# Optimization experiments

Hardware: AMD Instinct MI355X
Metric: run time of the kernel (lower is better)

Reference implementation:

```python
import jax, jax.numpy as jnp
import numpy as np

B = 131072   # batch of state samples
H = 512      # hidden width of reconstructed subnets
EPS_DIAG = 0.1  # diagonal regularization ensuring M is invertible


def setup_inputs() -> dict:
    key = jax.random.key(0)
    ks = jax.random.split(key, 20)
    f32 = jnp.float32
    inp = {
        "q":      jax.random.normal(ks[0], (B, 3), dtype=f32),
        "q_dot":  jax.random.normal(ks[1], (B, 3), dtype=f32),
        "s":      jax.random.normal(ks[2], (B, 3), dtype=f32),
        "s_Ddot": jax.random.normal(ks[3], (B, 3), dtype=f32),
        "tau":    jax.random.normal(ks[4], (B, 3), dtype=f32),
        # viscous / coulomb friction coefficients (f_v1..3, f_c1..3)
        "fv": jnp.full((3,), 0.05, dtype=f32),
        "fc": jnp.full((3,), 0.05, dtype=f32),
        # Mass net: 3 -> H -> 9
        "W1m": jax.random.normal(ks[5], (3, H), dtype=f32) * 0.1,
        "b1m": jnp.zeros((H,), dtype=f32),
        "W2m": jax.random.normal(ks[6], (H, 9), dtype=f32) * 0.05,
        "b2m": jnp.zeros((9,), dtype=f32),
        # Gravity net: 3 -> H -> 3
        "W1g": jax.random.normal(ks[7], (3, H), dtype=f32) * 0.1,
        "b1g": jnp.zeros((H,), dtype=f32),
        "W2g": jax.random.normal(ks[8], (H, 3), dtype=f32) * 0.05,
        "b2g": jnp.zeros((3,), dtype=f32),
        # KAB net: concat(q, s, s_Ddot)=9 -> H -> 3
        "W1k": jax.random.normal(ks[9], (9, H), dtype=f32) * 0.1,
        "b1k": jnp.zeros((H,), dtype=f32),
        "W2k": jax.random.normal(ks[10], (H, 3), dtype=f32) * 0.05,
        "b2k": jnp.zeros((3,), dtype=f32),
    }
    return inp


def reference(q, q_dot, s, s_Ddot, tau, fv, fc,
              W1m, b1m, W2m, b2m,
              W1g, b1g, W2g, b2g,
              W1k, b1k, W2k, b2k) -> jnp.ndarray:
    # Mass matrix net -> [B,3,3], made SPD-ish so inv(M) is well defined
    hm = jnp.tanh(q @ W1m + b1m)                       # [B,H]
    Mraw = (hm @ W2m + b2m).reshape(-1, 3, 3)          # [B,3,3]
    M = jnp.einsum('bij,bkj->bik', Mraw, Mraw) + EPS_DIAG * jnp.eye(3, dtype=q.dtype)

    # Gravity net -> [B,3]
    hg = jnp.tanh(q @ W1g + b1g)
    G = hg @ W2g + b2g

    # KAB net on concat(q, s, s_Ddot) -> [B,3]
    x = jnp.concatenate([q, s, s_Ddot], axis=-1)       # [B,9]
    hk = jnp.tanh(x @ W1k + b1k)
    KAB = hk @ W2k + b2k

    # diag(fv) @ q_dot and diag(fc) @ sign(q_dot) are elementwise scalings
    rhs = -G + KAB - fv * q_dot - fc * jnp.sign(q_dot) + tau  # [B,3]

    # q_Ddot = inv(M) @ rhs  (solve is the same math, fewer ops)
    q_Ddot = jnp.linalg.solve(M, rhs[..., None]).squeeze(-1)  # [B,3]
    return q_Ddot
```

## Files before the change

kernel.cpp:

```cpp
#include <hip/hip_runtime.h>
#include <math.h>

#define HDIM 512
#define NCH1 96
#define NCH2 48
#define EPS_DIAG 0.1f

typedef __fp16 h2 __attribute__((ext_vector_type(2)));
typedef __fp16 h8 __attribute__((ext_vector_type(8)));
typedef float f32x4 __attribute__((ext_vector_type(4)));
typedef unsigned int u32x4 __attribute__((ext_vector_type(4)));

__device__ __forceinline__ h2 f2h2(float a, float b) {
    return __builtin_amdgcn_cvt_pkrtz(a, b);
}

__device__ __forceinline__ h2 tanh2(h2 x) {
    const h2 HI = {(__fp16)2.0f,        (__fp16)2.0f};
    const h2 LO = {(__fp16)-2.0f,       (__fp16)-2.0f};
    const h2 C0 = {(__fp16)0.993654f,   (__fp16)0.993654f};
    const h2 C1 = {(__fp16)-0.29463f,   (__fp16)-0.29463f};
    const h2 C2 = {(__fp16)0.0695331f,  (__fp16)0.0695331f};
    const h2 C3 = {(__fp16)-0.00696328f,(__fp16)-0.00696328f};
    h2 t = __builtin_elementwise_min(__builtin_elementwise_max(x, LO), HI);
    h2 u = t * t;
    h2 p = __builtin_elementwise_fma(C3, u, C2);
    p = __builtin_elementwise_fma(p, u, C1);
    p = __builtin_elementwise_fma(p, u, C0);
    return t * p;
}

__device__ __forceinline__ float w1c_at(int k, int hid,
    const float* W1m, const float* b1m, const float* W1g, const float* b1g,
    const float* W1k, const float* b1k)
{
    if (hid < 512)  { if (k < 3) return W1m[k*HDIM + hid]; if (k == 9) return b1m[hid]; return 0.f; }
    if (hid < 1024) { const int h = hid - 512;
                      if (k < 3) return W1g[k*HDIM + h];  if (k == 9) return b1g[h];  return 0.f; }
    const int h = hid - 1024;
    if (k < 9) return W1k[k*HDIM + h]; if (k == 9) return b1k[h]; return 0.f;
}

__global__ void pack_frags(const float* __restrict__ W1m, const float* __restrict__ b1m,
                           const float* __restrict__ W2m,
                           const float* __restrict__ W1g, const float* __restrict__ b1g,
                           const float* __restrict__ W2g,
                           const float* __restrict__ W1k, const float* __restrict__ b1k,
                           const float* __restrict__ W2k,
                           __fp16* __restrict__ frag)
{
    const int tid = blockIdx.x * blockDim.x + threadIdx.x;
    if (tid >= (NCH1 + NCH2) * 64) return;
    const int c = tid >> 6, l = tid & 63;
    const int m = l & 15, kq = l >> 4;
    __fp16* dst = frag + (size_t)tid * 8;
    if (c < NCH1) {
        const int t = c >> 1, phase = c & 1;
        const int hid = 32*t + 8*(m >> 2) + (m & 3) + 4*phase;
        #pragma unroll
        for (int j = 0; j < 8; ++j) {
            const int k = kq*8 + j;
            dst[j] = (__fp16)((k < 10) ? w1c_at(k, hid, W1m, b1m, W1g, b1g, W1k, b1k) : 0.f);
        }
    } else {
        const int t = c - NCH1;
        #pragma unroll
        for (int j = 0; j < 8; ++j) {
            const int hid = 32*t + kq*8 + j;
            float v = 0.f;
            if (hid < 512)       { if (m < 9)             v = W2m[hid*9 + m]; }
            else if (hid < 1024) { if (m >= 9 && m < 12)  v = W2g[(hid-512)*3 + (m-9)]; }
            else                 { if (m >= 12 && m < 15) v = W2k[(hid-1024)*3 + (m-12)]; }
            dst[j] = (__fp16)v;
        }
    }
}

__global__ __launch_bounds__(256, 4) void dyn_kernel(
    const __fp16* __restrict__ frag,
    const float* __restrict__ q, const float* __restrict__ q_dot,
    const float* __restrict__ s, const float* __restrict__ s_Ddot,
    const float* __restrict__ tau,
    const float* __restrict__ fv, const float* __restrict__ fc,
    const float* __restrict__ b2m, const float* __restrict__ b2g,
    const float* __restrict__ b2k,
    float* __restrict__ out, int n)
{
    __shared__ float ebuf[4][32][20];

    const int lane = threadIdx.x & 63;
    const int w    = threadIdx.x >> 6;
    const int col  = lane & 15;
    const int quad = lane >> 4;
    const int base32 = (blockIdx.x * 4 + w) * 32;

    h8 ax0, ax1;
    {
        int sm = base32 + col; if (sm >= n) sm = n - 1;
        const float q0 = q[3*sm+0], q1 = q[3*sm+1], q2 = q[3*sm+2];
        const float s0 = s[3*sm+0], s1 = s[3*sm+1], s2 = s[3*sm+2];
        const float d0 = s_Ddot[3*sm+0], d1 = s_Ddot[3*sm+1], d2 = s_Ddot[3*sm+2];
        const bool z0 = (quad == 0), z1 = (quad == 1);
        ax0[0] = (__fp16)(z0 ? q0 : (z1 ? d2  : 0.f));
        ax0[1] = (__fp16)(z0 ? q1 : (z1 ? 1.f : 0.f));
        ax0[2] = (__fp16)(z0 ? q2 : 0.f);
        ax0[3] = (__fp16)(z0 ? s0 : 0.f);
        ax0[4] = (__fp16)(z0 ? s1 : 0.f);
        ax0[5] = (__fp16)(z0 ? s2 : 0.f);
        ax0[6] = (__fp16)(z0 ? d0 : 0.f);
        ax0[7] = (__fp16)(z0 ? d1 : 0.f);
    }
    {
        int sm = base32 + 16 + col; if (sm >= n) sm = n - 1;
        const float q0 = q[3*sm+0], q1 = q[3*sm+1], q2 = q[3*sm+2];
        const float s0 = s[3*sm+0], s1 = s[3*sm+1], s2 = s[3*sm+2];
        const float d0 = s_Ddot[3*sm+0], d1 = s_Ddot[3*sm+1], d2 = s_Ddot[3*sm+2];
        const bool z0 = (quad == 0), z1 = (quad == 1);
        ax1[0] = (__fp16)(z0 ? q0 : (z1 ? d2  : 0.f));
        ax1[1] = (__fp16)(z0 ? q1 : (z1 ? 1.f : 0.f));
        ax1[2] = (__fp16)(z0 ? q2 : 0.f);
        ax1[3] = (__fp16)(z0 ? s0 : 0.f);
        ax1[4] = (__fp16)(z0 ? s1 : 0.f);
        ax1[5] = (__fp16)(z0 ? s2 : 0.f);
        ax1[6] = (__fp16)(z0 ? d0 : 0.f);
        ax1[7] = (__fp16)(z0 ? d1 : 0.f);
    }

    const f32x4 zero4 = {0.f, 0.f, 0.f, 0.f};
    f32x4 acc0 = zero4, acc1 = zero4;

    const h8* p1 = (const h8*)frag + lane;
    const h8* p2 = (const h8*)frag + (size_t)NCH1 * 64 + lane;

#define BODY(W1A, W1B, W2V) do {                                              \
        f32x4 pa0 = __builtin_amdgcn_mfma_f32_16x16x32_f16((W1A), ax0, zero4, 0, 0, 0); \
        f32x4 pb0 = __builtin_amdgcn_mfma_f32_16x16x32_f16((W1B), ax0, zero4, 0, 0, 0); \
        f32x4 pa1 = __builtin_amdgcn_mfma_f32_16x16x32_f16((W1A), ax1, zero4, 0, 0, 0); \
        f32x4 pb1 = __builtin_amdgcn_mfma_f32_16x16x32_f16((W1B), ax1, zero4, 0, 0, 0); \
        u32x4 uv;                                                             \
        uv[0] = __builtin_bit_cast(unsigned int, tanh2(f2h2(pa0[0], pa0[1]))); \
        uv[1] = __builtin_bit_cast(unsigned int, tanh2(f2h2(pa0[2], pa0[3]))); \
        uv[2] = __builtin_bit_cast(unsigned int, tanh2(f2h2(pb0[0], pb0[1]))); \
        uv[3] = __builtin_bit_cast(unsigned int, tanh2(f2h2(pb0[2], pb0[3]))); \
        acc0 = __builtin_amdgcn_mfma_f32_16x16x32_f16((W2V), __builtin_bit_cast(h8, uv), acc0, 0, 0, 0); \
        uv[0] = __builtin_bit_cast(unsigned int, tanh2(f2h2(pa1[0], pa1[1]))); \
        uv[1] = __builtin_bit_cast(unsigned int, tanh2(f2h2(pa1[2], pa1[3]))); \
        uv[2] = __builtin_bit_cast(unsigned int, tanh2(f2h2(pb1[0], pb1[1]))); \
        uv[3] = __builtin_bit_cast(unsigned int, tanh2(f2h2(pb1[2], pb1[3]))); \
        acc1 = __builtin_amdgcn_mfma_f32_16x16x32_f16((W2V), __builtin_bit_cast(h8, uv), acc1, 0, 0, 0); \
    } while (0)

    h8 a0 = p1[0], b0 = p1[64], c0 = p2[0];
    int t = 0;
    for (; t < NCH2 - 2; t += 2) {
        h8 a1 = p1[128], b1 = p1[192], c1 = p2[64];
        p1 += 256; p2 += 128;
        BODY(a0, b0, c0);
        a0 = p1[0]; b0 = p1[64]; c0 = p2[0];
        BODY(a1, b1, c1);
    }
    {
        h8 a1 = p1[128], b1 = p1[192], c1 = p2[64];
        BODY(a0, b0, c0);
        BODY(a1, b1, c1);
    }
#undef BODY

    *(f32x4*)(&ebuf[w][col][4*quad])      = acc0;
    *(f32x4*)(&ebuf[w][16 + col][4*quad]) = acc1;
    asm volatile("s_waitcnt lgkmcnt(0)" ::: "memory");

    if (lane < 32) {
        const int i = base32 + lane;
        if (i < n) {
            const float* R = ebuf[w][lane];
            const float bM0 = R[0]  + b2m[0], bM1 = R[1]  + b2m[1], bM2 = R[2]  + b2m[2];
            const float bM3 = R[3]  + b2m[3], bM4 = R[4]  + b2m[4], bM5 = R[5]  + b2m[5];
            const float bM6 = R[6]  + b2m[6], bM7 = R[7]  + b2m[7], bM8 = R[8]  + b2m[8];
            const float bG0 = R[9]  + b2g[0], bG1 = R[10] + b2g[1], bG2 = R[11] + b2g[2];
            const float bK0 = R[12] + b2k[0], bK1 = R[13] + b2k[1], bK2 = R[14] + b2k[2];

            const float m00 = bM0*bM0 + bM1*bM1 + bM2*bM2 + EPS_DIAG;
            const float m01 = bM0*bM3 + bM1*bM4 + bM2*bM5;
            const float m02 = bM0*bM6 + bM1*bM7 + bM2*bM8;
            const float m11 = bM3*bM3 + bM4*bM4 + bM5*bM5 + EPS_DIAG;
            const float m12 = bM3*bM6 + bM4*bM7 + bM5*bM8;
            const float m22 = bM6*bM6 + bM7*bM7 + bM8*bM8 + EPS_DIAG;

            const float qd0 = q_dot[3*i+0], qd1 = q_dot[3*i+1], qd2 = q_dot[3*i+2];
            const float t0 = tau[3*i+0], t1 = tau[3*i+1], t2 = tau[3*i+2];
            const float fv0 = fv[0], fv1 = fv[1], fv2 = fv[2];
            const float fc0 = fc[0], fc1 = fc[1], fc2 = fc[2];
            const float sg0 = (qd0 > 0.f) ? 1.f : ((qd0 < 0.f) ? -1.f : 0.f);
            const float sg1 = (qd1 > 0.f) ? 1.f : ((qd1 < 0.f) ? -1.f : 0.f);
            const float sg2 = (qd2 > 0.f) ? 1.f : ((qd2 < 0.f) ? -1.f : 0.f);
            const float r0 = -bG0 + bK0 - fv0*qd0 - fc0*sg0 + t0;
            const float r1 = -bG1 + bK1 - fv1*qd1 - fc1*sg1 + t1;
            const float r2 = -bG2 + bK2 - fv2*qd2 - fc2*sg2 + t2;

            const float c00 = m11*m22 - m12*m12;
            const float c01 = m02*m12 - m01*m22;
            const float c02 = m01*m12 - m02*m11;
            const float det = m00*c00 + m01*c01 + m02*c02;
            const float idet = 1.0f / det;
            const float i11 = m00*m22 - m02*m02;
            const float i12 = m01*m02 - m00*m12;
            const float i22 = m00*m11 - m01*m01;

            out[3*i+0] = (c00*r0 + c01*r1 + c02*r2) * idet;
            out[3*i+1] = (c01*r0 + i11*r1 + i12*r2) * idet;
            out[3*i+2] = (c02*r0 + i12*r1 + i22*r2) * idet;
        }
    }
}

extern "C" void kernel_launch(void* const* d_in, const int* in_sizes, int n_in,
                              void* d_out, int out_size, void* d_ws, size_t ws_size,
                              hipStream_t stream) {
    const float* q      = (const float*)d_in[0];
    const float* q_dot  = (const float*)d_in[1];
    const float* s      = (const float*)d_in[2];
    const float* s_Ddot = (const float*)d_in[3];
    const float* tau    = (const float*)d_in[4];
    const float* fv     = (const float*)d_in[5];
    const float* fc     = (const float*)d_in[6];
    const float* W1m    = (const float*)d_in[7];
    const float* b1m    = (const float*)d_in[8];
    const float* W2m    = (const float*)d_in[9];
    const float* b2m    = (const float*)d_in[10];
    const float* W1g    = (const float*)d_in[11];
    const float* b1g    = (const float*)d_in[12];
    const float* W2g    = (const float*)d_in[13];
    const float* b2g    = (const float*)d_in[14];
    const float* W1k    = (const float*)d_in[15];
    const float* b1k    = (const float*)d_in[16];
    const float* W2k    = (const float*)d_in[17];
    const float* b2k    = (const float*)d_in[18];
    float* out = (float*)d_out;
    __fp16* frag = (__fp16*)d_ws;

    const int n = in_sizes[0] / 3;

    pack_frags<<<((NCH1 + NCH2) * 64 + 255) / 256, 256, 0, stream>>>(
        W1m, b1m, W2m, W1g, b1g, W2g, W1k, b1k, W2k, frag);

    const int blocks = (n + 127) / 128;
    dyn_kernel<<<blocks, 256, 0, stream>>>(frag, q, q_dot, s, s_Ddot, tau, fv, fc,
                                           b2m, b2g, b2k, out, n);
}
```

Measured before the change: 129.3 us.

## Split hidden dimension across wave pairs and reduce partial outputs via LDS

Each pair of waves now shares one 32-sample tile. Each wave in the pair processes half of the hidden chunks, and the two partial second-layer accumulators are summed through shared memory before the solve. Blocks now cover 64 samples instead of 128, so the grid doubles, and launch bounds are raised to 8 blocks per CU to shorten each wave's serial MFMA/tanh chain and raise parallelism. The cost is a __syncthreads, extra LDS traffic, a second input load per sample, and tighter register limits.

Measured after the change: 131.4 us. Within noise of the previous version (+1.6%).

```diff
diff --git a/kernel.cpp b/kernel.cpp
--- a/kernel.cpp
+++ b/kernel.cpp
@@ -4,6 +4,7 @@
 #define HDIM 512
 #define NCH1 96
 #define NCH2 48
+#define NCHH 24
 #define EPS_DIAG 0.1f
 
 typedef __fp16 h2 __attribute__((ext_vector_type(2)));
@@ -76,7 +77,7 @@
     }
 }
 
-__global__ __launch_bounds__(256, 4) void dyn_kernel(
+__global__ __launch_bounds__(256, 8) void dyn_kernel(
     const __fp16* __restrict__ frag,
     const float* __restrict__ q, const float* __restrict__ q_dot,
     const float* __restrict__ s, const float* __restrict__ s_Ddot,
@@ -86,13 +87,16 @@
     const float* __restrict__ b2k,
     float* __restrict__ out, int n)
 {
-    __shared__ float ebuf[4][32][20];
+    __shared__ float bufA[2][32][20];
+    __shared__ float bufB[2][32][20];
 
     const int lane = threadIdx.x & 63;
     const int w    = threadIdx.x >> 6;
+    const int pair = w >> 1;
+    const int half = w & 1;
     const int col  = lane & 15;
     const int quad = lane >> 4;
-    const int base32 = (blockIdx.x * 4 + w) * 32;
+    const int base32 = blockIdx.x * 64 + pair * 32;
 
     h8 ax0, ax1;
     {
@@ -129,8 +133,8 @@
     const f32x4 zero4 = {0.f, 0.f, 0.f, 0.f};
     f32x4 acc0 = zero4, acc1 = zero4;
 
-    const h8* p1 = (const h8*)frag + lane;
-    const h8* p2 = (const h8*)frag + (size_t)NCH1 * 64 + lane;
+    const h8* p1 = (const h8*)frag + lane + (size_t)half * (48 * 64);
+    const h8* p2 = (const h8*)frag + (size_t)NCH1 * 64 + lane + (size_t)half * (NCHH * 64);
 
 #define BODY(W1A, W1B, W2V) do {                                              \
         f32x4 pa0 = __builtin_amdgcn_mfma_f32_16x16x32_f16((W1A), ax0, zero4, 0, 0, 0); \
@@ -152,7 +156,7 @@
 
     h8 a0 = p1[0], b0 = p1[64], c0 = p2[0];
     int t = 0;
-    for (; t < NCH2 - 2; t += 2) {
+    for (; t < NCHH - 2; t += 2) {
         h8 a1 = p1[128], b1 = p1[192], c1 = p2[64];
         p1 += 256; p2 += 128;
         BODY(a0, b0, c0);
@@ -166,19 +170,33 @@
     }
 #undef BODY
 
-    *(f32x4*)(&ebuf[w][col][4*quad])      = acc0;
-    *(f32x4*)(&ebuf[w][16 + col][4*quad]) = acc1;
-    asm volatile("s_waitcnt lgkmcnt(0)" ::: "memory");
-
-    if (lane < 32) {
+    {
+        float (*mybuf)[32][20] = half ? bufB : bufA;
+        *(f32x4*)(&mybuf[pair][col][4*quad])      = acc0;
+        *(f32x4*)(&mybuf[pair][16 + col][4*quad]) = acc1;
+    }
+    __syncthreads();
+
+    if (half == 1 && lane < 32) {
         const int i = base32 + lane;
         if (i < n) {
-            const float* R = ebuf[w][lane];
-            const float bM0 = R[0]  + b2m[0], bM1 = R[1]  + b2m[1], bM2 = R[2]  + b2m[2];
-            const float bM3 = R[3]  + b2m[3], bM4 = R[4]  + b2m[4], bM5 = R[5]  + b2m[5];
-            const float bM6 = R[6]  + b2m[6], bM7 = R[7]  + b2m[7], bM8 = R[8]  + b2m[8];
-            const float bG0 = R[9]  + b2g[0], bG1 = R[10] + b2g[1], bG2 = R[11] + b2g[2];
-            const float bK0 = R[12] + b2k[0], bK1 = R[13] + b2k[1], bK2 = R[14] + b2k[2];
+            const float* RA = bufA[pair][lane];
+            const float* RB = bufB[pair][lane];
+            const float bM0 = RA[0]  + RB[0]  + b2m[0];
+            const float bM1 = RA[1]  + RB[1]  + b2m[1];
+            const float bM2 = RA[2]  + RB[2]  + b2m[2];
+            const float bM3 = RA[3]  + RB[3]  + b2m[3];
+            const float bM4 = RA[4]  + RB[4]  + b2m[4];
+            const float bM5 = RA[5]  + RB[5]  + b2m[5];
+            const float bM6 = RA[6]  + RB[6]  + b2m[6];
+            const float bM7 = RA[7]  + RB[7]  + b2m[7];
+            const float bM8 = RA[8]  + RB[8]  + b2m[8];
+            const float bG0 = RA[9]  + RB[9]  + b2g[0];
+            const float bG1 = RA[10] + RB[10] + b2g[1];
+            const float bG2 = RA[11] + RB[11] + b2g[2];
+            const float bK0 = RA[12] + RB[12] + b2k[0];
+            const float bK1 = RA[13] + RB[13] + b2k[1];
+            const float bK2 = RA[14] + RB[14] + b2k[2];
 
             const float m00 = bM0*bM0 + bM1*bM1 + bM2*bM2 + EPS_DIAG;
             const float m01 = bM0*bM3 + bM1*bM4 + bM2*bM5;
@@ -244,7 +262,7 @@
     pack_frags<<<((NCH1 + NCH2) * 64 + 255) / 256, 256, 0, stream>>>(
         W1m, b1m, W2m, W1g, b1g, W2g, W1k, b1k, W2k, frag);
 
-    const int blocks = (n + 127) / 128;
+    const int blocks = (n + 63) / 64;
     dyn_kernel<<<blocks, 256, 0, stream>>>(frag, q, q_dot, s, s_Ddot, tau, fv, fc,
                                            b2m, b2g, b2k, out, n);
 }
```
